# Kernel tuning notes

Measured on AMD Instinct MI355X. Metric: run time of the kernel, lower is better.

Reference implementation:

```python
import jax, jax.numpy as jnp
import numpy as np


def setup_inputs() -> dict:
    key = jax.random.key(0)
    ks = jax.random.split(key, 4)
    B, C, H, W = 8, 64, 256, 256
    return {
        "x": jax.random.normal(ks[0], (B, C, H, W), jnp.float32),
        "fc_w": jax.random.normal(ks[1], (C, C), jnp.float32) / np.sqrt(C).astype(np.float32),
        "fc_b": jnp.zeros((C,), jnp.float32),
        "conv1_w": jax.random.normal(ks[2], (2,), jnp.float32),  # [mean_ch, max_ch] of 1x1 conv
        "conv1_b": jnp.zeros((1,), jnp.float32),
        "conv2_w": jax.random.normal(ks[3], (2,), jnp.float32),
        "conv2_b": jnp.zeros((1,), jnp.float32),
        "size": 4,
    }


def reference(x, fc_w, fc_b, conv1_w, conv1_b, conv2_w, conv2_b, size):
    B, C, H, W = x.shape
    s = size
    h, w = H // s, W // s
    # unfold (non-overlapping) -> [B, L, C, s*s], L = h*w, patch pixels row-major
    p = x.reshape(B, C, h, s, w, s).transpose(0, 2, 4, 1, 3, 5).reshape(B, h * w, C, s * s)
    # channel attention: max over patch pixels -> fc -> sigmoid
    m = jax.nn.sigmoid(jnp.max(p, axis=3) @ fc_w.T + fc_b)  # [B, L, C]
    p = p * m[..., None]
    # spatial-in-patch attention: (mean, max) over channel axis -> 1x1 conv(2->1) -> sigmoid
    g1 = jax.nn.sigmoid(
        conv1_w[0] * jnp.mean(p, axis=2, keepdims=True)
        + conv1_w[1] * jnp.max(p, axis=2, keepdims=True)
        + conv1_b[0]
    )  # [B, L, 1, s*s]
    p = p * g1
    # fold back to [B, C, H, W]
    y = p.reshape(B, h, w, C, s, s).transpose(0, 3, 1, 4, 2, 5).reshape(B, C, H, W)
    # per-patch gating: (mean, max) over all C*s*s values of each patch
    yb = y.reshape(B, C, h, s, w, s)
    mx = jnp.max(yb, axis=(1, 3, 5))   # [B, h, w]
    mn = jnp.mean(yb, axis=(1, 3, 5))  # [B, h, w]
    g2 = jax.nn.sigmoid(conv2_w[0] * mn + conv2_w[1] * mx + conv2_b[0])
    g2 = jnp.repeat(jnp.repeat(g2, s, axis=1), s, axis=2)  # [B, H, W]
    return y * g2[:, None, :, :]
```

## Files before the change

### kernel.cpp

```cpp
#include <hip/hip_runtime.h>
#include <math.h>

constexpr int Bc = 8, Cc = 64, Hc = 256, Wc = 256, Sc = 4;
constexpr int NPATCH = Bc * (Hc / Sc) * (Wc / Sc);
constexpr int TP = 8;

constexpr int RP = 36;
constexpr int CP = 4 * RP + 4;
constexpr int TILE_F = Cc * CP;

constexpr int FCW_P   = 66;
constexpr int FCW_OFF = 0;
constexpr int PIX_P   = 68;
constexpr int PIX_OFF = Cc * FCW_P;
constexpr int PIX_W   = 16 * PIX_P;
static_assert(PIX_OFF + 4 * PIX_W <= TILE_F, "overlay must fit inside tile");

__device__ __forceinline__ float sigmoidf_(float v) {
    return 1.0f / (1.0f + __expf(-v));
}

__global__ __launch_bounds__(256, 4)
void ciam_kernel(const float* __restrict__ x,
                 const float* __restrict__ fc_w,
                 const float* __restrict__ fc_b,
                 const float* __restrict__ c1w,
                 const float* __restrict__ c1b,
                 const float* __restrict__ c2w,
                 const float* __restrict__ c2b,
                 float* __restrict__ out)
{
    __shared__ __align__(16) float S[TILE_F];
    __shared__ __align__(16) float maxbuf[TP][64];

    const int tid  = threadIdx.x;
    const int gid  = blockIdx.x;
    const int b    = gid >> 9;
    const int rem  = gid & 511;
    const int ph   = rem >> 3;
    const int pwg  = rem & 7;
    const int col0 = pwg * 32;

    float4 tl[8];
    #pragma unroll
    for (int i = 0; i < 8; ++i) {
        const int u = i * 256 + tid;
        const int seg = u >> 3, c_ = seg >> 2, r_ = seg & 3, j4 = (u & 7) << 2;
        tl[i] = *reinterpret_cast<const float4*>(
            x + (((size_t)(b * Cc + c_) * Hc + (ph * Sc + r_)) * Wc + col0 + j4));
    }
    float4 wl[4];
    #pragma unroll
    for (int i = 0; i < 4; ++i) {
        const int u = i * 256 + tid;
        const int row = u >> 4, jf = (u & 15) << 2;
        wl[i] = *reinterpret_cast<const float4*>(fc_w + row * 64 + jf);
    }
    const float fb  = fc_b[tid & 63];
    const float w10 = c1w[0], w11 = c1w[1], b1 = c1b[0];
    const float w20 = c2w[0], w21 = c2w[1], b2 = c2b[0];

    #pragma unroll
    for (int i = 0; i < 8; ++i) {
        const int u = i * 256 + tid;
        const int seg = u >> 3, c_ = seg >> 2, r_ = seg & 3, j4 = (u & 7) << 2;
        *reinterpret_cast<float4*>(&S[c_ * CP + r_ * RP + j4]) = tl[i];
    }
    __syncthreads();

    const int wave = tid >> 6, lane = tid & 63, c = lane;
    const int p0 = wave * 2;

    float v[2][16];
    #pragma unroll
    for (int pi = 0; pi < 2; ++pi) {
        const float* tp = &S[c * CP + (p0 + pi) * 4];
        #pragma unroll
        for (int r = 0; r < 4; ++r) {
            const float4 q4 = *reinterpret_cast<const float4*>(tp + r * RP);
            v[pi][r*4+0] = q4.x; v[pi][r*4+1] = q4.y;
            v[pi][r*4+2] = q4.z; v[pi][r*4+3] = q4.w;
        }
    }

    float mx0 = -3.4e38f, mx1 = -3.4e38f;
    #pragma unroll
    for (int t = 0; t < 16; ++t) {
        mx0 = fmaxf(mx0, v[0][t]);
        mx1 = fmaxf(mx1, v[1][t]);
    }
    maxbuf[p0][c]     = mx0;
    maxbuf[p0 + 1][c] = mx1;
    __syncthreads();

    #pragma unroll
    for (int i = 0; i < 4; ++i) {
        const int u = i * 256 + tid;
        const int row = u >> 4, jf = (u & 15) << 2;
        float* fd = &S[FCW_OFF + row * FCW_P + jf];
        fd[0] = wl[i].x; fd[1] = wl[i].y; fd[2] = wl[i].z; fd[3] = wl[i].w;
    }
    __syncthreads();

    const float* wrow = &S[FCW_OFF + c * FCW_P];
    const float* m0r  = maxbuf[p0];
    const float* m1r  = maxbuf[p0 + 1];
    float a0 = fb, a1 = fb;
    #pragma unroll 8
    for (int k2 = 0; k2 < 32; ++k2) {
        const float2 wv = *reinterpret_cast<const float2*>(wrow + 2 * k2);
        const float2 q0 = *reinterpret_cast<const float2*>(m0r + 2 * k2);
        const float2 q1 = *reinterpret_cast<const float2*>(m1r + 2 * k2);
        a0 = fmaf(wv.x, q0.x, a0); a0 = fmaf(wv.y, q0.y, a0);
        a1 = fmaf(wv.x, q1.x, a1); a1 = fmaf(wv.y, q1.y, a1);
    }
    const float m0 = sigmoidf_(a0), m1 = sigmoidf_(a1);
    #pragma unroll
    for (int t = 0; t < 16; ++t) { v[0][t] *= m0; v[1][t] *= m1; }

    float* PB = &S[PIX_OFF + wave * PIX_W];
    const int a_ = lane >> 2, q_ = lane & 3;
    const float* pbr = PB + a_ * PIX_P + q_ * 16;

    #pragma unroll
    for (int pi = 0; pi < 2; ++pi) {
        #pragma unroll
        for (int t = 0; t < 16; ++t)
            PB[t * PIX_P + c] = v[pi][t];
        __asm__ volatile("s_waitcnt lgkmcnt(0)" ::: "memory");

        float s = 0.f, mxp = -3.4e38f;
        #pragma unroll
        for (int t4 = 0; t4 < 4; ++t4) {
            const float4 u4 = *reinterpret_cast<const float4*>(pbr + 4 * t4);
            s += (u4.x + u4.y) + (u4.z + u4.w);
            mxp = fmaxf(mxp, fmaxf(fmaxf(u4.x, u4.y), fmaxf(u4.z, u4.w)));
        }
        s += __shfl_xor(s, 1);
        s += __shfl_xor(s, 2);
        mxp = fmaxf(mxp, __shfl_xor(mxp, 1));
        mxp = fmaxf(mxp, __shfl_xor(mxp, 2));
        const float g1 = sigmoidf_(w10 * (s * (1.f / 64.f)) + w11 * mxp + b1);

        float ts = g1 * s, tm = g1 * mxp;
        #pragma unroll
        for (int off = 4; off <= 32; off <<= 1) {
            ts += __shfl_xor(ts, off);
            tm  = fmaxf(tm, __shfl_xor(tm, off));
        }
        const float g2 = sigmoidf_(w20 * (ts * (1.f / 1024.f)) + w21 * tm + b2);

        #pragma unroll
        for (int t = 0; t < 16; ++t)
            v[pi][t] *= __shfl(g1, t << 2) * g2;
    }
    __syncthreads();

    #pragma unroll
    for (int pi = 0; pi < 2; ++pi) {
        float* tp = &S[c * CP + (p0 + pi) * 4];
        #pragma unroll
        for (int r = 0; r < 4; ++r) {
            float4 o;
            o.x = v[pi][r*4+0]; o.y = v[pi][r*4+1];
            o.z = v[pi][r*4+2]; o.w = v[pi][r*4+3];
            *reinterpret_cast<float4*>(tp + r * RP) = o;
        }
    }
    __syncthreads();

    #pragma unroll
    for (int i = 0; i < 8; ++i) {
        const int u = i * 256 + tid;
        const int seg = u >> 3, c_ = seg >> 2, r_ = seg & 3, j4 = (u & 7) << 2;
        const float* ts = &S[c_ * CP + r_ * RP + j4];
        float4 o;
        o.x = ts[0]; o.y = ts[1]; o.z = ts[2]; o.w = ts[3];
        *reinterpret_cast<float4*>(
            out + (((size_t)(b * Cc + c_) * Hc + (ph * Sc + r_)) * Wc + col0 + j4)) = o;
    }
}

extern "C" void kernel_launch(void* const* d_in, const int* in_sizes, int n_in,
                              void* d_out, int out_size, void* d_ws, size_t ws_size,
                              hipStream_t stream) {
    const float* x    = (const float*)d_in[0];
    const float* fc_w = (const float*)d_in[1];
    const float* fc_b = (const float*)d_in[2];
    const float* c1w  = (const float*)d_in[3];
    const float* c1b  = (const float*)d_in[4];
    const float* c2w  = (const float*)d_in[5];
    const float* c2b  = (const float*)d_in[6];

    float* out = (float*)d_out;
    ciam_kernel<<<NPATCH / TP, 256, 0, stream>>>(x, fc_w, fc_b, c1w, c1b, c2w, c2b, out);
}
```

Before: 251.3 us.

## Swizzle shared-memory tile layout, use readlane for FC maxes, raise occupancy

Measured after the change: 277.3 us. 10.3% more time.

```diff
diff --git a/kernel.cpp b/kernel.cpp
--- a/kernel.cpp
+++ b/kernel.cpp
@@ -5,22 +5,18 @@
 constexpr int NPATCH = Bc * (Hc / Sc) * (Wc / Sc);
 constexpr int TP = 8;
 
-constexpr int RP = 36;
-constexpr int CP = 4 * RP + 4;
-constexpr int TILE_F = Cc * CP;
-
-constexpr int FCW_P   = 66;
+constexpr int TILE_F = Cc * 128;
 constexpr int FCW_OFF = 0;
-constexpr int PIX_P   = 68;
-constexpr int PIX_OFF = Cc * FCW_P;
-constexpr int PIX_W   = 16 * PIX_P;
-static_assert(PIX_OFF + 4 * PIX_W <= TILE_F, "overlay must fit inside tile");
+constexpr int PIX_OFF = 4096;
 
 __device__ __forceinline__ float sigmoidf_(float v) {
     return 1.0f / (1.0f + __expf(-v));
 }
+__device__ __forceinline__ float rdlane(float v, int l) {
+    return __int_as_float(__builtin_amdgcn_readlane(__float_as_int(v), l));
+}
 
-__global__ __launch_bounds__(256, 4)
+__global__ __launch_bounds__(256, 5)
 void ciam_kernel(const float* __restrict__ x,
                  const float* __restrict__ fc_w,
                  const float* __restrict__ fc_b,
@@ -31,7 +27,6 @@
                  float* __restrict__ out)
 {
     __shared__ __align__(16) float S[TILE_F];
-    __shared__ __align__(16) float maxbuf[TP][64];
 
     const int tid  = threadIdx.x;
     const int gid  = blockIdx.x;
@@ -45,9 +40,9 @@
     #pragma unroll
     for (int i = 0; i < 8; ++i) {
         const int u = i * 256 + tid;
-        const int seg = u >> 3, c_ = seg >> 2, r_ = seg & 3, j4 = (u & 7) << 2;
+        const int seg = u >> 3, c_ = seg >> 2, r_ = seg & 3, J = u & 7;
         tl[i] = *reinterpret_cast<const float4*>(
-            x + (((size_t)(b * Cc + c_) * Hc + (ph * Sc + r_)) * Wc + col0 + j4));
+            x + (((size_t)(b * Cc + c_) * Hc + (ph * Sc + r_)) * Wc + col0 + J * 4));
     }
     float4 wl[4];
     #pragma unroll
@@ -63,23 +58,25 @@
     #pragma unroll
     for (int i = 0; i < 8; ++i) {
         const int u = i * 256 + tid;
-        const int seg = u >> 3, c_ = seg >> 2, r_ = seg & 3, j4 = (u & 7) << 2;
-        *reinterpret_cast<float4*>(&S[c_ * CP + r_ * RP + j4]) = tl[i];
+        const int seg = u >> 3, c_ = seg >> 2, r_ = seg & 3, J = u & 7;
+        const int e = J * 16 + r_ * 4;
+        *reinterpret_cast<float4*>(&S[c_ * 128 + (e ^ ((c_ & 7) << 2))]) = tl[i];
     }
     __syncthreads();
 
     const int wave = tid >> 6, lane = tid & 63, c = lane;
     const int p0 = wave * 2;
+    const int ckey = (c & 7) << 2;
 
     float v[2][16];
     #pragma unroll
     for (int pi = 0; pi < 2; ++pi) {
-        const float* tp = &S[c * CP + (p0 + pi) * 4];
         #pragma unroll
-        for (int r = 0; r < 4; ++r) {
-            const float4 q4 = *reinterpret_cast<const float4*>(tp + r * RP);
-            v[pi][r*4+0] = q4.x; v[pi][r*4+1] = q4.y;
-            v[pi][r*4+2] = q4.z; v[pi][r*4+3] = q4.w;
+        for (int o = 0; o < 4; ++o) {
+            const float4 q4 = *reinterpret_cast<const float4*>(
+                &S[c * 128 + (((p0 + pi) * 16 + o * 4) ^ ckey)]);
+            v[pi][o*4+0] = q4.x; v[pi][o*4+1] = q4.y;
+            v[pi][o*4+2] = q4.z; v[pi][o*4+3] = q4.w;
         }
     }
 
@@ -89,50 +86,51 @@
         mx0 = fmaxf(mx0, v[0][t]);
         mx1 = fmaxf(mx1, v[1][t]);
     }
-    maxbuf[p0][c]     = mx0;
-    maxbuf[p0 + 1][c] = mx1;
     __syncthreads();
 
     #pragma unroll
     for (int i = 0; i < 4; ++i) {
         const int u = i * 256 + tid;
         const int row = u >> 4, jf = (u & 15) << 2;
-        float* fd = &S[FCW_OFF + row * FCW_P + jf];
-        fd[0] = wl[i].x; fd[1] = wl[i].y; fd[2] = wl[i].z; fd[3] = wl[i].w;
+        *reinterpret_cast<float4*>(
+            &S[FCW_OFF + row * 64 + (jf ^ ((row & 7) << 2))]) = wl[i];
     }
     __syncthreads();
 
-    const float* wrow = &S[FCW_OFF + c * FCW_P];
-    const float* m0r  = maxbuf[p0];
-    const float* m1r  = maxbuf[p0 + 1];
     float a0 = fb, a1 = fb;
-    #pragma unroll 8
-    for (int k2 = 0; k2 < 32; ++k2) {
-        const float2 wv = *reinterpret_cast<const float2*>(wrow + 2 * k2);
-        const float2 q0 = *reinterpret_cast<const float2*>(m0r + 2 * k2);
-        const float2 q1 = *reinterpret_cast<const float2*>(m1r + 2 * k2);
-        a0 = fmaf(wv.x, q0.x, a0); a0 = fmaf(wv.y, q0.y, a0);
-        a1 = fmaf(wv.x, q1.x, a1); a1 = fmaf(wv.y, q1.y, a1);
+    #pragma unroll
+    for (int k4 = 0; k4 < 64; k4 += 4) {
+        const float4 wv = *reinterpret_cast<const float4*>(
+            &S[FCW_OFF + c * 64 + (k4 ^ ckey)]);
+        a0 = fmaf(wv.x, rdlane(mx0, k4 + 0), a0);
+        a0 = fmaf(wv.y, rdlane(mx0, k4 + 1), a0);
+        a0 = fmaf(wv.z, rdlane(mx0, k4 + 2), a0);
+        a0 = fmaf(wv.w, rdlane(mx0, k4 + 3), a0);
+        a1 = fmaf(wv.x, rdlane(mx1, k4 + 0), a1);
+        a1 = fmaf(wv.y, rdlane(mx1, k4 + 1), a1);
+        a1 = fmaf(wv.z, rdlane(mx1, k4 + 2), a1);
+        a1 = fmaf(wv.w, rdlane(mx1, k4 + 3), a1);
     }
     const float m0 = sigmoidf_(a0), m1 = sigmoidf_(a1);
     #pragma unroll
     for (int t = 0; t < 16; ++t) { v[0][t] *= m0; v[1][t] *= m1; }
 
-    float* PB = &S[PIX_OFF + wave * PIX_W];
+    float* PB = &S[PIX_OFF + wave * 1024];
     const int a_ = lane >> 2, q_ = lane & 3;
-    const float* pbr = PB + a_ * PIX_P + q_ * 16;
+    const int akey = (a_ & 7) << 2;
 
     #pragma unroll
     for (int pi = 0; pi < 2; ++pi) {
         #pragma unroll
         for (int t = 0; t < 16; ++t)
-            PB[t * PIX_P + c] = v[pi][t];
+            PB[t * 64 + (c ^ ((t & 7) << 2))] = v[pi][t];
         __asm__ volatile("s_waitcnt lgkmcnt(0)" ::: "memory");
 
         float s = 0.f, mxp = -3.4e38f;
         #pragma unroll
-        for (int t4 = 0; t4 < 4; ++t4) {
-            const float4 u4 = *reinterpret_cast<const float4*>(pbr + 4 * t4);
+        for (int m = 0; m < 4; ++m) {
+            const float4 u4 = *reinterpret_cast<const float4*>(
+                &PB[a_ * 64 + ((q_ * 16 + m * 4) ^ akey)]);
             s += (u4.x + u4.y) + (u4.z + u4.w);
             mxp = fmaxf(mxp, fmaxf(fmaxf(u4.x, u4.y), fmaxf(u4.z, u4.w)));
         }
@@ -158,13 +156,13 @@
 
     #pragma unroll
     for (int pi = 0; pi < 2; ++pi) {
-        float* tp = &S[c * CP + (p0 + pi) * 4];
         #pragma unroll
-        for (int r = 0; r < 4; ++r) {
-            float4 o;
-            o.x = v[pi][r*4+0]; o.y = v[pi][r*4+1];
-            o.z = v[pi][r*4+2]; o.w = v[pi][r*4+3];
-            *reinterpret_cast<float4*>(tp + r * RP) = o;
+        for (int o = 0; o < 4; ++o) {
+            float4 q4;
+            q4.x = v[pi][o*4+0]; q4.y = v[pi][o*4+1];
+            q4.z = v[pi][o*4+2]; q4.w = v[pi][o*4+3];
+            *reinterpret_cast<float4*>(
+                &S[c * 128 + (((p0 + pi) * 16 + o * 4) ^ ckey)]) = q4;
         }
     }
     __syncthreads();
@@ -172,12 +170,13 @@
     #pragma unroll
     for (int i = 0; i < 8; ++i) {
         const int u = i * 256 + tid;
-        const int seg = u >> 3, c_ = seg >> 2, r_ = seg & 3, j4 = (u & 7) << 2;
-        const float* ts = &S[c_ * CP + r_ * RP + j4];
+        const int seg = u >> 3, c_ = seg >> 2, r_ = seg & 3, J = u & 7;
+        const int e = J * 16 + r_ * 4;
+        const float* ts = &S[c_ * 128 + (e ^ ((c_ & 7) << 2))];
         float4 o;
         o.x = ts[0]; o.y = ts[1]; o.z = ts[2]; o.w = ts[3];
         *reinterpret_cast<float4*>(
-            out + (((size_t)(b * Cc + c_) * Hc + (ph * Sc + r_)) * Wc + col0 + j4)) = o;
+            out + (((size_t)(b * Cc + c_) * Hc + (ph * Sc + r_)) * Wc + col0 + J * 4)) = o;
     }
 }
 
```
